# Kernel optimization log

Measured on AMD Instinct MI355X. Metric: run time of the kernel, lower is better.

The kernel has to match this reference:

```python
import jax, jax.numpy as jnp
import numpy as np

B, T, D = 4, 2048, 1024
N_HEAD, HEAD_SIZE = 16, 64
MASK_FILL = 1e-9  # faithful to original: masked_fill uses 1e-9, not -inf


def setup_inputs() -> dict:
    key = jax.random.key(0)
    k1, k2, k3 = jax.random.split(key, 3)
    x = jax.random.normal(k1, (B, T, D), dtype=jnp.float32)
    # per-head qkv projection weights, stacked: [n_head, d_model, 3*head_size]
    W_qkv = jax.random.normal(k2, (N_HEAD, D, 3 * HEAD_SIZE), dtype=jnp.float32) * (D ** -0.5)
    # output projection [d_model, d_model] (x @ W_out convention)
    W_out = jax.random.normal(k3, (D, D), dtype=jnp.float32) * (D ** -0.5)
    return {"x": x, "W_qkv": W_qkv, "W_out": W_out}


def reference(x, W_qkv, W_out):
    Bv, Tv, C = x.shape
    # qkv for all heads at once: [B, H, T, 3*head_size]
    qkv = jnp.einsum("btc,hcf->bhtf", x, W_qkv)
    q, k, v = jnp.split(qkv, 3, axis=-1)  # each [B, H, T, head_size]
    # NOTE: original scales by C**-0.5 where C = d_model (not head_size)
    scores = jnp.einsum("bhtd,bhsd->bhts", q, k) * (C ** -0.5)
    causal = jnp.tril(jnp.ones((Tv, Tv), dtype=bool))
    # faithful bug: masked positions set to 1e-9 before softmax (not -inf)
    scores = jnp.where(causal, scores, MASK_FILL)
    attn = jax.nn.softmax(scores, axis=-1)
    out_heads = jnp.einsum("bhts,bhsd->bhtd", attn, v)  # [B, H, T, head_size]
    mha = out_heads.transpose(0, 2, 1, 3).reshape(Bv, Tv, C)  # concat heads
    return mha @ W_out
```

## Files before the change

kernel.cpp:

```cpp
#include <hip/hip_runtime.h>

typedef unsigned short u16;
typedef __attribute__((ext_vector_type(8))) short short8;
typedef __attribute__((ext_vector_type(4))) short short4v;
typedef __attribute__((ext_vector_type(4))) float f32x4;

#define B_  4
#define T_  2048
#define D_  1024
#define H_  16
#define HS_ 64
#define M_    (B_ * T_)
#define NQKV_ (H_ * 3 * HS_)
#define NTILE_ (T_ / 64)
#define LOG2E_ 1.44269504088896340736f

__device__ __forceinline__ u16 f2bf(float f) {
  union { float f; unsigned u; } v; v.f = f;
  unsigned u = v.u;
  return (u16)((u + 0x7FFFu + ((u >> 16) & 1u)) >> 16);
}
__device__ __forceinline__ float bf2f(u16 h) {
  union { unsigned u; float f; } v; v.u = ((unsigned)h) << 16; return v.f;
}
__device__ __forceinline__ unsigned pkbf(float lo, float hi) {
  unsigned r;
  asm("v_cvt_pk_bf16_f32 %0, %1, %2" : "=v"(r) : "v"(lo), "v"(hi));
  return r;
}
__device__ __forceinline__ float exp2fast(float x) {
  float r;
  asm("v_exp_f32 %0, %1" : "=v"(r) : "v"(x));
  return r;
}
__device__ __forceinline__ void gload16(const u16* g, u16* l) {
  __builtin_amdgcn_global_load_lds(
      (const __attribute__((address_space(1))) void*)g,
      (__attribute__((address_space(3))) void*)l, 16, 0, 0);
}

__global__ void k_cvt_x(const float* __restrict__ x, u16* __restrict__ o, int n4) {
  int i = blockIdx.x * 256 + threadIdx.x;
  if (i < n4) {
    float4 v = ((const float4*)x)[i];
    short4v d;
    d[0] = (short)f2bf(v.x); d[1] = (short)f2bf(v.y);
    d[2] = (short)f2bf(v.z); d[3] = (short)f2bf(v.w);
    ((short4v*)o)[i] = d;
  }
}

__global__ void k_transpose_cvt(const float* __restrict__ in, u16* __restrict__ out,
                                int R, int C, long sIn, long sOut) {
  __shared__ float tile[32][33];
  int h = blockIdx.z;
  const float* src = in + (long)h * sIn;
  u16* dst = out + (long)h * sOut;
  int r0 = blockIdx.y * 32, c0 = blockIdx.x * 32;
  int tx = threadIdx.x, ty = threadIdx.y;
  #pragma unroll
  for (int i = 0; i < 32; i += 8) {
    int r = r0 + ty + i, c = c0 + tx;
    tile[ty + i][tx] = (r < R && c < C) ? src[(long)r * C + c] : 0.f;
  }
  __syncthreads();
  #pragma unroll
  for (int i = 0; i < 32; i += 8) {
    int c = c0 + ty + i, r = r0 + tx;
    if (c < C && r < R) dst[(long)c * R + r] = f2bf(tile[tx][ty + i]);
  }
}

template<int MODE>
__global__ __launch_bounds__(256) void k_gemm(
    const u16* __restrict__ A, const u16* __restrict__ Bt,
    u16* __restrict__ Oq, u16* __restrict__ Ok, u16* __restrict__ Ov,
    float* __restrict__ Of, int K) {
  __shared__ __align__(16) u16 smem[32768];
  int mt = blockIdx.x, nt = blockIdx.y;
  int tid = threadIdx.x;
  int wid = tid >> 6, lane = tid & 63;
  int lr = lane & 15, lg = lane >> 4;
  int mw = (wid >> 1) * 64, nw = (wid & 1) * 64;
  const u16* srcA[4]; const u16* srcB[4];
  int dstOff[4];
  #pragma unroll
  for (int l = 0; l < 4; l++) {
    int c = l * 256 + wid * 64 + lane;
    int r = c >> 3, q = c & 7;
    int qs = q ^ (r & 7);
    srcA[l] = A  + (long)(mt * 128 + r) * K + qs * 8;
    srcB[l] = Bt + (long)(nt * 128 + r) * K + qs * 8;
    dstOff[l] = (l * 256 + wid * 64) * 8;
  }
  const int rsw = (lr & 7);
  f32x4 acc[4][4] = {};
  const int nIter = K / 64;

#define STAGE_G(bb, k0) do {                       \
    u16* ab_ = smem + (bb) * 16384;                \
    gload16(srcA[0] + (k0), ab_ + dstOff[0]);      \
    gload16(srcA[1] + (k0), ab_ + dstOff[1]);      \
    gload16(srcA[2] + (k0), ab_ + dstOff[2]);      \
    gload16(srcA[3] + (k0), ab_ + dstOff[3]);      \
    u16* bb_ = ab_ + 8192;                         \
    gload16(srcB[0] + (k0), bb_ + dstOff[0]);      \
    gload16(srcB[1] + (k0), bb_ + dstOff[1]);      \
    gload16(srcB[2] + (k0), bb_ + dstOff[2]);      \
    gload16(srcB[3] + (k0), bb_ + dstOff[3]); } while (0)

  STAGE_G(0, 0);
  __syncthreads();
  for (int t = 0; t < nIter; t++) {
    int cur = t & 1;
    if (t + 1 < nIter) STAGE_G(cur ^ 1, (t + 1) * 64);
    const u16* As = smem + cur * 16384;
    const u16* Bs = As + 8192;
    #pragma unroll
    for (int kk = 0; kk < 2; kk++) {
      const int fc = ((kk * 4 + lg) ^ rsw) << 3;
      short8 af[4], bf[4];
      #pragma unroll
      for (int i = 0; i < 4; i++)
        af[i] = *(const short8*)(As + (mw + i * 16 + lr) * 64 + fc);
      #pragma unroll
      for (int i = 0; i < 4; i++)
        bf[i] = *(const short8*)(Bs + (nw + i * 16 + lr) * 64 + fc);
      #pragma unroll
      for (int i = 0; i < 4; i++)
        #pragma unroll
        for (int j = 0; j < 4; j++)
          acc[i][j] = __builtin_amdgcn_mfma_f32_16x16x32_bf16(af[i], bf[j], acc[i][j], 0, 0, 0);
    }
    __syncthreads();
  }
#undef STAGE_G

  if constexpr (MODE == 0) {
    u16* Cs = smem;
    #pragma unroll
    for (int j = 0; j < 4; j++) {
      int fbase = (nt * 128 + nw + j * 16) % 192;
      float sc = (fbase < 64) ? (0.03125f * LOG2E_) : 1.0f;
      #pragma unroll
      for (int i = 0; i < 4; i++) {
        int row = mw + i * 16 + lg * 4;
        int col = nw + j * 16 + lr;
        #pragma unroll
        for (int r = 0; r < 4; r++)
          Cs[(row + r) * 128 + col] = f2bf(acc[i][j][r] * sc);
      }
    }
    __syncthreads();
    #pragma unroll
    for (int p5 = 0; p5 < 8; p5++) {
      int idx = p5 * 2048 + tid * 8;
      int row = idx >> 7, col = idx & 127;
      short8 v = *(const short8*)(Cs + row * 128 + col);
      int m = mt * 128 + row;
      int n0 = nt * 128 + col;
      int b = m >> 11, t = m & (T_ - 1);
      int h = n0 / 192, f = n0 % 192;
      long o = (((long)(b * H_ + h)) * T_ + t) * HS_;
      u16* dst = (f < 64) ? (Oq + o + f) : (f < 128) ? (Ok + o + f - 64) : (Ov + o + f - 128);
      *(short8*)dst = v;
    }
  } else {
    #pragma unroll
    for (int i = 0; i < 4; i++) {
      #pragma unroll
      for (int j = 0; j < 4; j++) {
        int mbase = mt * 128 + mw + i * 16 + lg * 4;
        int n     = nt * 128 + nw + j * 16 + lr;
        #pragma unroll
        for (int r = 0; r < 4; r++)
          Of[(long)(mbase + r) * D_ + n] = acc[i][j][r];
      }
    }
  }
}

__global__ void k_transpose_v(const u16* __restrict__ V, u16* __restrict__ Vp,
                              float* __restrict__ Partial) {
  __shared__ u16 tile[64][65];
  __shared__ float psum[4][64];
  int bh = blockIdx.z;
  int jt = blockIdx.x;
  int t0 = jt * 64;
  int tx = threadIdx.x & 63, ty = threadIdx.x >> 6;
  const u16* src = V + (long)bh * T_ * HS_;
  u16* dtile = Vp + (((long)bh * NTILE_) + jt) * 64 * 64;
  #pragma unroll
  for (int i = 0; i < 64; i += 4)
    tile[ty + i][tx] = src[(long)(t0 + ty + i) * HS_ + tx];
  __syncthreads();
  int pos = ((tx >> 2) & 3) * 16 + ((tx >> 4) & 3) * 4 + (tx & 3);
  #pragma unroll
  for (int i = 0; i < 64; i += 4)
    dtile[(ty + i) * 64 + pos] = tile[tx][ty + i];
  float s = 0.f;
  #pragma unroll
  for (int i = 0; i < 16; i++)
    s += bf2f(tile[ty * 16 + i][tx]);
  psum[ty][tx] = s;
  __syncthreads();
  if (threadIdx.x < 64)
    Partial[((long)bh * NTILE_ + jt) * HS_ + threadIdx.x] =
        psum[0][threadIdx.x] + psum[1][threadIdx.x] + psum[2][threadIdx.x] + psum[3][threadIdx.x];
}

__global__ void k_vscan(const float* __restrict__ Partial, float* __restrict__ Suf) {
  int bh = blockIdx.x;
  int d = threadIdx.x;
  const float* Pb = Partial + (long)bh * NTILE_ * HS_;
  float* Sb = Suf + (long)bh * (NTILE_ + 1) * HS_;
  float acc = 0.f;
  Sb[NTILE_ * HS_ + d] = 0.f;
  for (int j = NTILE_ - 1; j >= 0; j--) {
    acc += Pb[j * HS_ + d];
    Sb[j * HS_ + d] = acc;
  }
}

__global__ __launch_bounds__(512, 2) void k_attn(
    const u16* __restrict__ Q, const u16* __restrict__ Kc,
    const u16* __restrict__ Vp, const float* __restrict__ Suf,
    u16* __restrict__ Mha) {
  __shared__ __align__(16) u16 Ks[2][64 * 64];
  __shared__ __align__(16) u16 Vs[2][64 * 64];
  int bh = blockIdx.x;
  int st = 7 - (int)blockIdx.y;
  int b = bh >> 4, h = bh & 15;
  int tid = threadIdx.x, wid = tid >> 6, lane = tid & 63;
  int lr = lane & 15, lg = lane >> 4;
  const u16* Qb = Q  + (long)bh * T_ * HS_;
  const u16* Kb = Kc + (long)bh * T_ * HS_;
  const u16* Vb = Vp + (long)bh * T_ * HS_;
  union U8 { unsigned u[4]; short8 s; };
  const short8 vone = { (short)0x3F80, (short)0x3F80, (short)0x3F80, (short)0x3F80,
                        (short)0x3F80, (short)0x3F80, (short)0x3F80, (short)0x3F80 };
  int srow = tid >> 3;
  int schunk = (tid & 7) ^ (srow & 7);
  const u16* kSrc = Kb + srow * 64 + schunk * 8;
  const u16* vSrc = Vb + srow * 64 + schunk * 8;
  const int r7 = lr & 7;
  const int kc0 = (lg ^ r7) << 3, kc1 = ((4 + lg) ^ r7) << 3;
  const int vc0 = ((2 * lg) ^ r7) << 3, vc1 = ((2 * lg + 1) ^ r7) << 3;

  int q0w = st * 256 + wid * 32;
  short8 qf[2][2];
  #pragma unroll
  for (int g = 0; g < 2; g++) {
    const u16* qp = Qb + (long)(q0w + g * 16 + lr) * HS_;
    qf[g][0] = *(const short8*)(qp + lg * 8);
    qf[g][1] = *(const short8*)(qp + 32 + lg * 8);
  }
  f32x4 accO[2][4] = {};
  f32x4 accL[2] = {};
  const int blkJ = 4 * st + 3;
  const int myJ  = 4 * st + (wid >> 1);
  gload16(kSrc, &Ks[0][wid * 512]);
  gload16(vSrc, &Vs[0][wid * 512]);
  __syncthreads();
  for (int jt = 0; jt <= blkJ; jt++) {
    int cur = jt & 1;
    if (jt < blkJ) {
      long off = (long)(jt + 1) * 4096;
      gload16(kSrc + off, &Ks[cur ^ 1][wid * 512]);
      gload16(vSrc + off, &Vs[cur ^ 1][wid * 512]);
    }
    if (jt <= myJ) {
      int j0 = jt * 64;
      const bool diag = (jt == myJ);
      const u16* Kl = Ks[cur];
      const u16* Vl = Vs[cur];
      f32x4 s4[2][4];
      #pragma unroll
      for (int fn = 0; fn < 4; fn++) {
        const u16* krow = Kl + (fn * 16 + lr) * 64;
        short8 kb0 = *(const short8*)(krow + kc0);
        short8 kb1 = *(const short8*)(krow + kc1);
        #pragma unroll
        for (int g = 0; g < 2; g++) {
          f32x4 z = {};
          z = __builtin_amdgcn_mfma_f32_16x16x32_bf16(kb0, qf[g][0], z, 0, 0, 0);
          z = __builtin_amdgcn_mfma_f32_16x16x32_bf16(kb1, qf[g][1], z, 0, 0, 0);
          s4[g][fn] = z;
        }
      }
      U8 pa[2][2];
      #pragma unroll
      for (int g = 0; g < 2; g++) {
        int qrow = q0w + g * 16 + lr;
        float p[4][4];
        #pragma unroll
        for (int fn = 0; fn < 4; fn++) {
          #pragma unroll
          for (int r = 0; r < 4; r++) {
            float v = s4[g][fn][r];
            if (diag) {
              int s = j0 + fn * 16 + lg * 4 + r;
              v = (s <= qrow) ? v : 0.0f;
            }
            p[fn][r] = exp2fast(v);
          }
        }
        pa[g][0].u[0] = pkbf(p[0][0], p[0][1]); pa[g][0].u[1] = pkbf(p[0][2], p[0][3]);
        pa[g][0].u[2] = pkbf(p[1][0], p[1][1]); pa[g][0].u[3] = pkbf(p[1][2], p[1][3]);
        pa[g][1].u[0] = pkbf(p[2][0], p[2][1]); pa[g][1].u[1] = pkbf(p[2][2], p[2][3]);
        pa[g][1].u[2] = pkbf(p[3][0], p[3][1]); pa[g][1].u[3] = pkbf(p[3][2], p[3][3]);
        accL[g] = __builtin_amdgcn_mfma_f32_16x16x32_bf16(pa[g][0].s, vone, accL[g], 0, 0, 0);
        accL[g] = __builtin_amdgcn_mfma_f32_16x16x32_bf16(pa[g][1].s, vone, accL[g], 0, 0, 0);
      }
      #pragma unroll
      for (int fd = 0; fd < 4; fd++) {
        const u16* vrow = Vl + (fd * 16 + lr) * 64;
        U8 vb0, vb1;
        vb0.s = *(const short8*)(vrow + vc0);
        vb1.s = *(const short8*)(vrow + vc1);
        #pragma unroll
        for (int g = 0; g < 2; g++) {
          accO[g][fd] = __builtin_amdgcn_mfma_f32_16x16x32_bf16(pa[g][0].s, vb0.s, accO[g][fd], 0, 0, 0);
          accO[g][fd] = __builtin_amdgcn_mfma_f32_16x16x32_bf16(pa[g][1].s, vb1.s, accO[g][fd], 0, 0, 0);
        }
      }
    }
    __syncthreads();
  }
  int nmask = T_ - (myJ + 1) * 64;
  const float* sufp = Suf + ((long)bh * (NTILE_ + 1) + (myJ + 1)) * HS_;
  float sufv[4];
  #pragma unroll
  for (int fd = 0; fd < 4; fd++) sufv[fd] = sufp[fd * 16 + lr];
  #pragma unroll
  for (int g = 0; g < 2; g++) {
    #pragma unroll
    for (int fd = 0; fd < 4; fd++) {
      #pragma unroll
      for (int r = 0; r < 4; r++) {
        int trow = q0w + g * 16 + lg * 4 + r;
        float o = (accO[g][fd][r] + sufv[fd]) / (accL[g][r] + (float)nmask);
        Mha[((long)(b * T_ + trow)) * D_ + h * HS_ + fd * 16 + lr] = f2bf(o);
      }
    }
  }
}

extern "C" void kernel_launch(void* const* d_in, const int* in_sizes, int n_in,
                              void* d_out, int out_size, void* d_ws, size_t ws_size,
                              hipStream_t stream) {
  const float* x    = (const float*)d_in[0];
  const float* wqkv = (const float*)d_in[1];
  const float* wout = (const float*)d_in[2];
  float* out = (float*)d_out;

  char* p = (char*)d_ws;
  u16* Xb    = (u16*)p; p += (size_t)M_ * D_ * 2;
  u16* WqkvT = (u16*)p; p += (size_t)NQKV_ * D_ * 2;
  u16* WoutT = (u16*)p; p += (size_t)D_ * D_ * 2;
  u16* Qw  = (u16*)p; p += (size_t)B_ * H_ * T_ * HS_ * 2;
  u16* Kw  = (u16*)p; p += (size_t)B_ * H_ * T_ * HS_ * 2;
  u16* Vw  = (u16*)p; p += (size_t)B_ * H_ * T_ * HS_ * 2;
  u16* Vpw = (u16*)p; p += (size_t)B_ * H_ * T_ * HS_ * 2;
  u16* Mha = (u16*)p; p += (size_t)M_ * D_ * 2;
  float* Suf = (float*)p; p += (size_t)B_ * H_ * (NTILE_ + 1) * HS_ * 4;
  float* Part = (float*)p; p += (size_t)B_ * H_ * NTILE_ * HS_ * 4;

  k_cvt_x<<<dim3(M_ * D_ / 4 / 256), dim3(256), 0, stream>>>(x, Xb, M_ * D_ / 4);
  k_transpose_cvt<<<dim3(192 / 32, D_ / 32, H_), dim3(32, 8), 0, stream>>>(
      wqkv, WqkvT, D_, 192, (long)D_ * 192, (long)192 * D_);
  k_transpose_cvt<<<dim3(D_ / 32, D_ / 32, 1), dim3(32, 8), 0, stream>>>(
      wout, WoutT, D_, D_, 0, 0);
  k_gemm<0><<<dim3(M_ / 128, NQKV_ / 128), dim3(256), 0, stream>>>(
      Xb, WqkvT, Qw, Kw, Vw, nullptr, D_);
  k_transpose_v<<<dim3(T_ / 64, 1, B_ * H_), dim3(256), 0, stream>>>(Vw, Vpw, Part);
  k_vscan<<<dim3(B_ * H_), dim3(64), 0, stream>>>(Part, Suf);
  k_attn<<<dim3(B_ * H_, 8), dim3(512), 0, stream>>>(Qw, Kw, Vpw, Suf, Mha);
  k_gemm<1><<<dim3(M_ / 128, D_ / 128), dim3(256), 0, stream>>>(
      Mha, WoutT, nullptr, nullptr, nullptr, out, D_);
}
```

Measured before the change: 159.4 us.

## Interleave A/B tile prefetch with split MFMA phases in GEMM main loop

Splits the next-tile global-to-LDS prefetch into separate A and B halves and issues each before one of the two k-substeps. Each substep loads its fragments, then hits an explicit s_barrier and a scheduling barrier, and runs its MFMAs at raised wave priority. The goal is to spread memory issue across the compute phases and keep waves in lockstep so MFMA work overlaps the loads. In exchange it adds extra barriers per iteration, which could stall waves.

```diff
diff --git a/kernel.cpp b/kernel.cpp
--- a/kernel.cpp
+++ b/kernel.cpp
@@ -97,28 +97,29 @@
   f32x4 acc[4][4] = {};
   const int nIter = K / 64;
 
-#define STAGE_G(bb, k0) do {                       \
+#define STAGE_A(bb, k0) do {                       \
     u16* ab_ = smem + (bb) * 16384;                \
     gload16(srcA[0] + (k0), ab_ + dstOff[0]);      \
     gload16(srcA[1] + (k0), ab_ + dstOff[1]);      \
     gload16(srcA[2] + (k0), ab_ + dstOff[2]);      \
-    gload16(srcA[3] + (k0), ab_ + dstOff[3]);      \
-    u16* bb_ = ab_ + 8192;                         \
+    gload16(srcA[3] + (k0), ab_ + dstOff[3]); } while (0)
+#define STAGE_B(bb, k0) do {                       \
+    u16* bb_ = smem + (bb) * 16384 + 8192;         \
     gload16(srcB[0] + (k0), bb_ + dstOff[0]);      \
     gload16(srcB[1] + (k0), bb_ + dstOff[1]);      \
     gload16(srcB[2] + (k0), bb_ + dstOff[2]);      \
     gload16(srcB[3] + (k0), bb_ + dstOff[3]); } while (0)
 
-  STAGE_G(0, 0);
+  STAGE_A(0, 0);
+  STAGE_B(0, 0);
   __syncthreads();
   for (int t = 0; t < nIter; t++) {
     int cur = t & 1;
-    if (t + 1 < nIter) STAGE_G(cur ^ 1, (t + 1) * 64);
     const u16* As = smem + cur * 16384;
     const u16* Bs = As + 8192;
-    #pragma unroll
-    for (int kk = 0; kk < 2; kk++) {
-      const int fc = ((kk * 4 + lg) ^ rsw) << 3;
+    if (t + 1 < nIter) STAGE_A(cur ^ 1, (t + 1) * 64);
+    {
+      const int fc = (lg ^ rsw) << 3;
       short8 af[4], bf[4];
       #pragma unroll
       for (int i = 0; i < 4; i++)
@@ -126,15 +127,40 @@
       #pragma unroll
       for (int i = 0; i < 4; i++)
         bf[i] = *(const short8*)(Bs + (nw + i * 16 + lr) * 64 + fc);
+      __builtin_amdgcn_s_barrier();
+      __builtin_amdgcn_sched_barrier(0);
+      __builtin_amdgcn_s_setprio(1);
       #pragma unroll
       for (int i = 0; i < 4; i++)
         #pragma unroll
         for (int j = 0; j < 4; j++)
           acc[i][j] = __builtin_amdgcn_mfma_f32_16x16x32_bf16(af[i], bf[j], acc[i][j], 0, 0, 0);
+      __builtin_amdgcn_s_setprio(0);
+    }
+    if (t + 1 < nIter) STAGE_B(cur ^ 1, (t + 1) * 64);
+    {
+      const int fc = ((4 + lg) ^ rsw) << 3;
+      short8 af[4], bf[4];
+      #pragma unroll
+      for (int i = 0; i < 4; i++)
+        af[i] = *(const short8*)(As + (mw + i * 16 + lr) * 64 + fc);
+      #pragma unroll
+      for (int i = 0; i < 4; i++)
+        bf[i] = *(const short8*)(Bs + (nw + i * 16 + lr) * 64 + fc);
+      __builtin_amdgcn_s_barrier();
+      __builtin_amdgcn_sched_barrier(0);
+      __builtin_amdgcn_s_setprio(1);
+      #pragma unroll
+      for (int i = 0; i < 4; i++)
+        #pragma unroll
+        for (int j = 0; j < 4; j++)
+          acc[i][j] = __builtin_amdgcn_mfma_f32_16x16x32_bf16(af[i], bf[j], acc[i][j], 0, 0, 0);
+      __builtin_amdgcn_s_setprio(0);
     }
     __syncthreads();
   }
-#undef STAGE_G
+#undef STAGE_A
+#undef STAGE_B
 
   if constexpr (MODE == 0) {
     u16* Cs = smem;
```

Result: slower. 163.5 us (+2.6%).
